# Kernel optimization log

Hardware: AMD Instinct MI355X
Metric: run time of the kernel (lower is better)

Reference implementation:

```python
import jax, jax.numpy as jnp
import numpy as np

B, L, D, H, E, R, FF, K = 4, 1024, 1024, 16, 8, 64, 4096, 2
DH = D // H
EPS = 1e-5
SCALING = 2.0


def layer_norm(x, g, b):
    m = jnp.mean(x, axis=-1, keepdims=True)
    v = jnp.mean(jnp.square(x - m), axis=-1, keepdims=True)
    return (x - m) * jax.lax.rsqrt(v + EPS) * g + b


def setup_inputs() -> dict:
    key = jax.random.key(0)
    ks = jax.random.split(key, 16)
    s = 0.02
    return {
        "hidden_states": jax.random.normal(ks[0], (B, L, D), dtype=jnp.float32),
        "wq": jax.random.normal(ks[1], (D, D), dtype=jnp.float32) * s,
        "wk": jax.random.normal(ks[2], (D, D), dtype=jnp.float32) * s,
        "wv": jax.random.normal(ks[3], (D, D), dtype=jnp.float32) * s,
        "wo": jax.random.normal(ks[4], (D, D), dtype=jnp.float32) * s,
        "bq": jnp.zeros((D,), jnp.float32),
        "bk": jnp.zeros((D,), jnp.float32),
        "bv": jnp.zeros((D,), jnp.float32),
        "bo": jnp.zeros((D,), jnp.float32),
        "ln1_g": jnp.ones((D,), jnp.float32),
        "ln1_b": jnp.zeros((D,), jnp.float32),
        "w1": jax.random.normal(ks[5], (D, FF), dtype=jnp.float32) * s,
        "b1": jnp.zeros((FF,), jnp.float32),
        "w2": jax.random.normal(ks[6], (FF, D), dtype=jnp.float32) * s,
        "b2": jnp.zeros((D,), jnp.float32),
        "ln2_g": jnp.ones((D,), jnp.float32),
        "ln2_b": jnp.zeros((D,), jnp.float32),
        # adapter: dense1 D -> E*R, per-expert dense2 R -> D, gate D -> E
        "adp_w1": jax.random.normal(ks[7], (D, E * R), dtype=jnp.float32) * s,
        "adp_b1": jnp.zeros((E * R,), jnp.float32),
        "adp_w2": jax.random.normal(ks[8], (E, R, D), dtype=jnp.float32) * s,
        "adp_b2": jnp.zeros((E, D), jnp.float32),
        "gate_w": jax.random.normal(ks[9], (D, E), dtype=jnp.float32) * s,
        "gate_b": jnp.zeros((E,), jnp.float32),
    }


def reference(hidden_states, wq, wk, wv, wo, bq, bk, bv, bo, ln1_g, ln1_b,
              w1, b1, w2, b2, ln2_g, ln2_b,
              adp_w1, adp_b1, adp_w2, adp_b2, gate_w, gate_b):
    x = hidden_states
    # --- Roberta self-attention ---
    q = (x @ wq + bq).reshape(B, L, H, DH)
    k = (x @ wk + bk).reshape(B, L, H, DH)
    v = (x @ wv + bv).reshape(B, L, H, DH)
    scores = jnp.einsum("bqhd,bkhd->bhqk", q, k) / jnp.sqrt(jnp.float32(DH))
    probs = jax.nn.softmax(scores, axis=-1)
    ctx = jnp.einsum("bhqk,bkhd->bqhd", probs, v).reshape(B, L, D)
    attn_out = layer_norm(ctx @ wo + bo + x, ln1_g, ln1_b)

    # --- FFN (intermediate + output) ---
    inter = jax.nn.gelu(attn_out @ w1 + b1, approximate=False)
    layer_out = layer_norm(inter @ w2 + b2 + attn_out, ln2_g, ln2_b)

    # --- LoRA_MD_Adapter with NaiveGate (dense compute all experts, then combine) ---
    h = jax.nn.gelu(attn_out @ adp_w1 + adp_b1, approximate=False)  # [B,L,E*R]
    h = h.reshape(B, L, E, R)
    adp = jnp.einsum("bler,erd->bled", h, adp_w2) + adp_b2  # [B,L,E,D]
    logits = attn_out @ gate_w + gate_b  # [B,L,E]
    topv, topi = jax.lax.top_k(logits, K)  # [B,L,K]
    gate_score = jax.nn.softmax(topv, axis=-1)  # [B,L,K]
    # LoRA_MD combine: weight ALL per-expert outputs by top-k softmax scores
    # scattered to the selected experts, then sum over experts.
    picked = jnp.take_along_axis(adp, topi[..., None], axis=2)  # [B,L,K,D]
    adp_out = jnp.sum(picked * gate_score[..., None], axis=2) * SCALING  # [B,L,D]

    return layer_out + adp_out
```

## Files before the change

kernel.cpp:

```cpp
#include <hip/hip_runtime.h>
#include <cstddef>
#include <cstdint>

#define B_   4
#define L_   1024
#define D_   1024
#define H_   16
#define DH_  64
#define E_   8
#define R_   64
#define FF_  4096
#define NTOK (B_ * L_)

typedef __attribute__((ext_vector_type(8))) short bf16x8;
typedef __attribute__((ext_vector_type(4))) float f32x4;
typedef unsigned short us;

__device__ __forceinline__ float gelu_f(float x) {
  return 0.5f * x * (1.0f + erff(x * 0.7071067811865476f));
}

__device__ __forceinline__ us bf16_of(float f) {
  union { float f; uint32_t u; } x; x.f = f;
  uint32_t r = x.u + 0x7FFFu + ((x.u >> 16) & 1u);
  return (us)(r >> 16);
}
__device__ __forceinline__ float f32_of(us h) {
  union { uint32_t u; float f; } x; x.u = ((uint32_t)h) << 16;
  return x.f;
}
__device__ __forceinline__ void split_hl(float v, us& hi, us& lo) {
  hi = bf16_of(v);
  lo = bf16_of(v - f32_of(hi));
}

__device__ __forceinline__ void glds16(const void* g, const void* l) {
  __builtin_amdgcn_global_load_lds(
      (const __attribute__((address_space(1))) unsigned int*)g,
      (__attribute__((address_space(3))) unsigned int*)l, 16, 0, 0);
}

__global__ __launch_bounds__(256)
void fhi(const float* __restrict__ X, us* __restrict__ Hh, int n4) {
  int i = blockIdx.x * 256 + threadIdx.x;
  if (i >= n4) return;
  float4 v = ((const float4*)X)[i];
  ushort4 h = {bf16_of(v.x), bf16_of(v.y), bf16_of(v.z), bf16_of(v.w)};
  ((ushort4*)Hh)[i] = h;
}

__global__ __launch_bounds__(256)
void bconcat(const float* __restrict__ a, const float* __restrict__ b,
             const float* __restrict__ c, float* __restrict__ o) {
  int i = blockIdx.x * 256 + threadIdx.x;
  if (i >= 3072) return;
  o[i] = (i < 1024) ? a[i] : (i < 2048 ? b[i - 1024] : c[i - 2048]);
}

__global__ __launch_bounds__(256)
void wsplit_t(const float* __restrict__ W, us* __restrict__ Th,
              us* __restrict__ Tl, int K, int N) {
  __shared__ float tile[64][65];
  const int k0 = blockIdx.y * 64, n0 = blockIdx.x * 64;
  const int t = threadIdx.x;
  const int r = t >> 4, c4 = (t & 15) * 4;
  #pragma unroll
  for (int p = 0; p < 4; ++p) {
    const int k = r + p * 16;
    *(float4*)&tile[k][c4] = *(const float4*)&W[(size_t)(k0 + k) * N + n0 + c4];
  }
  __syncthreads();
  #pragma unroll
  for (int p = 0; p < 4; ++p) {
    const int n = r + p * 16;
    float v0 = tile[c4 + 0][n], v1 = tile[c4 + 1][n];
    float v2 = tile[c4 + 2][n], v3 = tile[c4 + 3][n];
    ushort4 h, l;
    split_hl(v0, h.x, l.x); split_hl(v1, h.y, l.y);
    split_hl(v2, h.z, l.z); split_hl(v3, h.w, l.w);
    const size_t o = (size_t)(n0 + n) * K + k0 + c4;
    *(ushort4*)&Th[o] = h;
    *(ushort4*)&Tl[o] = l;
  }
}

template<int EPI>
__global__ __launch_bounds__(256, 2)
void gemm_mfma(const us* __restrict__ Ah, const us* __restrict__ Al,
               const us* __restrict__ Bh, const us* __restrict__ Bl,
               const float* __restrict__ bias,
               const float* __restrict__ ResF,
               float* __restrict__ Cf, int M, int N, int K) {
  __shared__ us sAh[128 * 32], sAl[128 * 32];
  __shared__ us sBh[128 * 32], sBl[128 * 32];

  const int t = threadIdx.x;
  const int lane = t & 63;
  const int wid = t >> 6;
  const int wm = wid >> 1, wn = wid & 1;

  const int nwgx = gridDim.x;
  const int nwg = nwgx * gridDim.y;
  const int idl = blockIdx.y * nwgx + blockIdx.x;
  const int swz = (idl & 7) * (nwg >> 3) + (idl >> 3);
  const int m0 = (swz / nwgx) * 128;
  const int n0 = (swz % nwgx) * 128;

  const int srow = wid * 32 + (lane >> 2);
  const int skoff = (lane & 3) * 8;

  f32x4 acc[4][4];
  #pragma unroll
  for (int i = 0; i < 4; ++i)
    #pragma unroll
    for (int j = 0; j < 4; ++j)
      acc[i][j] = (f32x4){0.f, 0.f, 0.f, 0.f};

  const int fr = lane & 15, fq = lane >> 4;

  for (int k0 = 0; k0 < K; k0 += 32) {
    __syncthreads();
    #pragma unroll
    for (int c = 0; c < 2; ++c) {
      const size_t ga = (size_t)(m0 + srow + c * 16) * K + k0 + skoff;
      const size_t gb = (size_t)(n0 + srow + c * 16) * K + k0 + skoff;
      const int ldso = (wid * 32 + c * 16) * 32;
      glds16(Ah + ga, &sAh[ldso]);
      glds16(Al + ga, &sAl[ldso]);
      glds16(Bh + gb, &sBh[ldso]);
      glds16(Bl + gb, &sBl[ldso]);
    }
    __syncthreads();

    bf16x8 ah[4], al[4], bh[4], bl[4];
    #pragma unroll
    for (int i = 0; i < 4; ++i) {
      const int ra = (wm * 64 + i * 16 + fr) * 32 + fq * 8;
      ah[i] = *(const bf16x8*)&sAh[ra];
      al[i] = *(const bf16x8*)&sAl[ra];
      const int rb = (wn * 64 + i * 16 + fr) * 32 + fq * 8;
      bh[i] = *(const bf16x8*)&sBh[rb];
      bl[i] = *(const bf16x8*)&sBl[rb];
    }
    #pragma unroll
    for (int i = 0; i < 4; ++i)
      #pragma unroll
      for (int j = 0; j < 4; ++j) {
        acc[i][j] = __builtin_amdgcn_mfma_f32_16x16x32_bf16(ah[i], bh[j], acc[i][j], 0, 0, 0);
        acc[i][j] = __builtin_amdgcn_mfma_f32_16x16x32_bf16(al[i], bh[j], acc[i][j], 0, 0, 0);
        acc[i][j] = __builtin_amdgcn_mfma_f32_16x16x32_bf16(ah[i], bl[j], acc[i][j], 0, 0, 0);
      }
  }

  float bcol[4];
  #pragma unroll
  for (int j = 0; j < 4; ++j) bcol[j] = bias[n0 + wn * 64 + j * 16 + fr];

  #pragma unroll
  for (int i = 0; i < 4; ++i) {
    #pragma unroll
    for (int r = 0; r < 4; ++r) {
      const int row = m0 + wm * 64 + i * 16 + fq * 4 + r;
      const size_t ro = (size_t)row * N;
      #pragma unroll
      for (int j = 0; j < 4; ++j) {
        const int col = n0 + wn * 64 + j * 16 + fr;
        float v = acc[i][j][r] + bcol[j];
        if (EPI == 1) {
          Cf[ro + col] = gelu_f(v);
        } else if (EPI == 2) {
          Cf[ro + col] = v + ResF[ro + col];
        } else {
          Cf[ro + col] = v;
        }
      }
    }
  }
}

template<int EPI>
__global__ __launch_bounds__(512, 2)
void gemm256(const us* __restrict__ Ah,
             const us* __restrict__ Bh, const us* __restrict__ Bl,
             const float* __restrict__ bias,
             float* __restrict__ Cf, us* __restrict__ Ch, us* __restrict__ Cl,
             us* __restrict__ Kh2, us* __restrict__ Kl2,
             us* __restrict__ Vh2, us* __restrict__ Vl2,
             int M, int N, int Kfull, int klen) {
  __shared__ us sm3[3][3][8192];

  const int t = threadIdx.x;
  const int lane = t & 63, wid = t >> 6;
  const int wm = wid >> 2, wn = wid & 3;
  const int fr = lane & 15, fq = lane >> 4;
  const int rsw8 = (fq ^ ((fr >> 1) & 3)) * 8;

  const int nx = N >> 8;
  const int idl = blockIdx.x + blockIdx.y * nx;
  const int xcd = idl & 7, jj = idl >> 3;
  const int band = (M >> 8) >> 3;
  const int m0 = (xcd * band + (jj % band)) << 8;
  const int n0 = (jj / band) << 8;
  const int koff = blockIdx.z * klen;

  const int srow = t >> 2;
  const int gchunk = (t & 3) ^ ((t >> 3) & 3);
  const int dso = srow * 32 + (t & 3) * 8;

  auto stage1 = [&](int buf, int kt, int idx) {
    const int stream = idx >> 1;
    const int half = idx & 1;
    const us* gp = (stream == 0) ? Ah : (stream == 1 ? Bh : Bl);
    const int rbase = ((stream == 0) ? m0 : n0) + half * 128 + srow;
    const size_t g = (size_t)rbase * Kfull + koff + kt * 32 + gchunk * 8;
    glds16(gp + g, &sm3[buf][stream][half * 4096 + dso]);
  };

  f32x4 acc[8][4];
  #pragma unroll
  for (int i = 0; i < 8; ++i)
    #pragma unroll
    for (int n = 0; n < 4; ++n) acc[i][n] = (f32x4){0.f, 0.f, 0.f, 0.f};

  #pragma unroll
  for (int idx = 0; idx < 6; ++idx) stage1(0, 0, idx);
  #pragma unroll
  for (int idx = 0; idx < 6; ++idx) stage1(1, 1, idx);

  const int nt = klen >> 5;
  for (int g = 0; g < nt; ++g) {
    const int cb = g % 3;
    if (g < nt - 1) { asm volatile("s_waitcnt vmcnt(6)" ::: "memory"); }
    else            { asm volatile("s_waitcnt vmcnt(0)" ::: "memory"); }
    __builtin_amdgcn_sched_barrier(0);
    __builtin_amdgcn_s_barrier();
    __builtin_amdgcn_sched_barrier(0);

    const us* sA  = sm3[cb][0];
    const us* sBh = sm3[cb][1];
    const us* sBl = sm3[cb][2];

    bf16x8 bhf[4], blf[4];
    #pragma unroll
    for (int n = 0; n < 4; ++n) {
      const int rb = (wn * 64 + n * 16 + fr) * 32 + rsw8;
      bhf[n] = *(const bf16x8*)&sBh[rb];
      blf[n] = *(const bf16x8*)&sBl[rb];
    }
    bf16x8 a_cur = *(const bf16x8*)&sA[(wm * 128 + fr) * 32 + rsw8];

    const bool pf = (g + 2 < nt);
    const int nb = (g + 2) % 3;

    #pragma unroll
    for (int i = 0; i < 8; ++i) {
      if (pf && i < 6) stage1(nb, g + 2, i);
      bf16x8 a_nxt;
      if (i < 7) {
        a_nxt = *(const bf16x8*)&sA[(wm * 128 + (i + 1) * 16 + fr) * 32 + rsw8];
        asm volatile("s_waitcnt lgkmcnt(1)" ::: "memory");
      } else {
        asm volatile("s_waitcnt lgkmcnt(0)" ::: "memory");
      }
      __builtin_amdgcn_sched_barrier(0);
      __builtin_amdgcn_s_setprio(1);
      #pragma unroll
      for (int n = 0; n < 4; ++n) {
        acc[i][n] = __builtin_amdgcn_mfma_f32_16x16x32_bf16(a_cur, bhf[n], acc[i][n], 0, 0, 0);
        acc[i][n] = __builtin_amdgcn_mfma_f32_16x16x32_bf16(a_cur, blf[n], acc[i][n], 0, 0, 0);
      }
      __builtin_amdgcn_s_setprio(0);
      if (i < 7) a_cur = a_nxt;
    }
  }

  if (EPI == 12) {
    float* pk = (blockIdx.z == 0) ? Cf :
                (blockIdx.z == 1) ? (float*)Kh2 :
                (blockIdx.z == 2) ? (float*)Kl2 : (float*)Vh2;
    #pragma unroll
    for (int i = 0; i < 8; ++i) {
      #pragma unroll
      for (int r = 0; r < 4; ++r) {
        const int row = m0 + wm * 128 + i * 16 + fq * 4 + r;
        const size_t ro = (size_t)row * N;
        #pragma unroll
        for (int n = 0; n < 4; ++n) {
          const int col = n0 + wn * 64 + n * 16 + fr;
          pk[ro + col] = acc[i][n][r];
        }
      }
    }
    return;
  }

  float bcol[4];
  #pragma unroll
  for (int n = 0; n < 4; ++n) bcol[n] = bias[n0 + wn * 64 + n * 16 + fr];

  if (EPI == 11) {
    #pragma unroll
    for (int i = 0; i < 8; ++i) {
      #pragma unroll
      for (int r = 0; r < 4; ++r) {
        const int row = m0 + wm * 128 + i * 16 + fq * 4 + r;
        const size_t ro = (size_t)row * N;
        #pragma unroll
        for (int n = 0; n < 4; ++n) {
          const int col = n0 + wn * 64 + n * 16 + fr;
          Ch[ro + col] = bf16_of(gelu_f(acc[i][n][r] + bcol[n]));
        }
      }
    }
    return;
  }

  {
    const int sel = n0 >> 10;
    if (sel < 2) {
      us* dh = (sel == 0) ? Ch : Kh2;
      us* dl = (sel == 0) ? Cl : Kl2;
      #pragma unroll
      for (int i = 0; i < 8; ++i) {
        #pragma unroll
        for (int r = 0; r < 4; ++r) {
          const int row = m0 + wm * 128 + i * 16 + fq * 4 + r;
          const size_t ro = (size_t)row * 1024;
          #pragma unroll
          for (int n = 0; n < 4; ++n) {
            const int c10 = (n0 & 1023) + wn * 64 + n * 16 + fr;
            float v = acc[i][n][r] + bcol[n];
            us h, l; split_hl(v, h, l);
            dh[ro + c10] = h; dl[ro + c10] = l;
          }
        }
      }
    } else {
      #pragma unroll
      for (int i = 0; i < 8; ++i) {
        #pragma unroll
        for (int n = 0; n < 4; ++n) {
          const int c10 = (n0 & 1023) + wn * 64 + n * 16 + fr;
          const int hh2 = c10 >> 6, dh = c10 & 63;
          const int row0 = m0 + wm * 128 + i * 16 + fq * 4;
          const int bb = row0 >> 10, ltok = row0 & 1023;
          ushort4 h4, l4;
          float v0 = acc[i][n][0] + bcol[n];
          float v1 = acc[i][n][1] + bcol[n];
          float v2 = acc[i][n][2] + bcol[n];
          float v3 = acc[i][n][3] + bcol[n];
          split_hl(v0, h4.x, l4.x); split_hl(v1, h4.y, l4.y);
          split_hl(v2, h4.z, l4.z); split_hl(v3, h4.w, l4.w);
          const size_t off = ((size_t)(bb * 16 + hh2) * 64 + dh) * L_ + ltok;
          *(ushort4*)&Vh2[off] = h4;
          *(ushort4*)&Vl2[off] = l4;
        }
      }
    }
  }
}

__global__ __launch_bounds__(256, 3)
void attn_mfma(const us* __restrict__ Qh, const us* __restrict__ Ql,
               const us* __restrict__ Kh, const us* __restrict__ Kl,
               const us* __restrict__ Vth, const us* __restrict__ Vtl,
               us* __restrict__ Oh, us* __restrict__ Ol) {
  const int raw = blockIdx.x + blockIdx.y * 16;
  const int hh = (raw & 7) + 8 * ((raw >> 3) >> 4);
  const int qq = (raw >> 3) & 15;
  const int b = hh >> 4, h = hh & 15;

  const int t = threadIdx.x;
  const int w = t >> 6, lane = t & 63;
  const int fr = lane & 15, g = lane >> 4;

  __shared__ __align__(16) unsigned char smem[51200];
  us* sKh = (us*)(smem);
  us* sKl = (us*)(smem + 8192);
  us* sVh = (us*)(smem + 16384);
  us* sVl = (us*)(smem + 24576);
  us* sPh = (us*)(smem + 32768);
  us* sPl = (us*)(smem + 41984);
  float* fb = (float*)smem;

  const int tok0 = b * L_ + qq * 64 + w * 16;
  bf16x8 qfh[2], qfl[2];
  #pragma unroll
  for (int ks = 0; ks < 2; ++ks) {
    const size_t qo = (size_t)(tok0 + fr) * D_ + h * 64 + ks * 32 + g * 8;
    qfh[ks] = *(const bf16x8*)&Qh[qo];
    qfl[ks] = *(const bf16x8*)&Ql[qo];
  }

  float m = -INFINITY, l = 0.0f;
  f32x4 ctx[4];
  #pragma unroll
  for (int i = 0; i < 4; ++i) ctx[i] = (f32x4){0.f, 0.f, 0.f, 0.f};

  for (int kt = 0; kt < 16; ++kt) {
    const int k0 = kt * 64;
    __syncthreads();
    #pragma unroll
    for (int p = 0; p < 2; ++p) {
      const int ci = w * 128 + p * 64 + lane;
      const int dbase = (w * 128 + p * 64) * 8;
      {
        const int ks = ci >> 8, rem = ci & 255, key = rem >> 2, sub = rem & 3;
        const size_t src = (size_t)(b * L_ + k0 + key) * D_ + h * 64 + ks * 32 + sub * 8;
        glds16(Kh + src, sKh + dbase);
        glds16(Kl + src, sKl + dbase);
      }
      {
        const int d = ci >> 3, c = ci & 7;
        const size_t src = (size_t)(hh * 64 + d) * L_ + k0 + ((c ^ (d & 7)) * 8);
        glds16(Vth + src, sVh + dbase);
        glds16(Vtl + src, sVl + dbase);
      }
    }
    __syncthreads();

    f32x4 accS[4];
    #pragma unroll
    for (int i = 0; i < 4; ++i) accS[i] = (f32x4){0.f, 0.f, 0.f, 0.f};
    #pragma unroll
    for (int ks = 0; ks < 2; ++ks) {
      #pragma unroll
      for (int i = 0; i < 4; ++i) {
        const int ra = (ks * 64 + i * 16 + fr) * 32 + g * 8;
        bf16x8 ah = *(const bf16x8*)&sKh[ra];
        bf16x8 al = *(const bf16x8*)&sKl[ra];
        accS[i] = __builtin_amdgcn_mfma_f32_16x16x32_bf16(ah, qfh[ks], accS[i], 0, 0, 0);
        accS[i] = __builtin_amdgcn_mfma_f32_16x16x32_bf16(al, qfh[ks], accS[i], 0, 0, 0);
        accS[i] = __builtin_amdgcn_mfma_f32_16x16x32_bf16(ah, qfl[ks], accS[i], 0, 0, 0);
      }
    }

    float sv[4][4];
    float mloc = -INFINITY;
    #pragma unroll
    for (int i = 0; i < 4; ++i)
      #pragma unroll
      for (int r = 0; r < 4; ++r) {
        sv[i][r] = accS[i][r] * 0.125f;
        mloc = fmaxf(mloc, sv[i][r]);
      }
    mloc = fmaxf(mloc, __shfl_xor(mloc, 16));
    mloc = fmaxf(mloc, __shfl_xor(mloc, 32));
    const float mnew = fmaxf(m, mloc);
    const float alpha = expf(m - mnew);
    float p[4][4];
    float lt = 0.f;
    #pragma unroll
    for (int i = 0; i < 4; ++i)
      #pragma unroll
      for (int r = 0; r < 4; ++r) {
        p[i][r] = expf(sv[i][r] - mnew);
        lt += p[i][r];
      }
    lt += __shfl_xor(lt, 16);
    lt += __shfl_xor(lt, 32);
    l = l * alpha + lt;
    m = mnew;
    #pragma unroll
    for (int i = 0; i < 4; ++i) {
      ctx[i][0] *= alpha; ctx[i][1] *= alpha;
      ctx[i][2] *= alpha; ctx[i][3] *= alpha;
    }

    #pragma unroll
    for (int i = 0; i < 4; ++i) {
      us h0 = bf16_of(p[i][0]), h1 = bf16_of(p[i][1]);
      us h2 = bf16_of(p[i][2]), h3 = bf16_of(p[i][3]);
      uint2 hv = {(uint32_t)h0 | ((uint32_t)h1 << 16),
                  (uint32_t)h2 | ((uint32_t)h3 << 16)};
      us l0 = bf16_of(p[i][0] - f32_of(h0)), l1 = bf16_of(p[i][1] - f32_of(h1));
      us l2 = bf16_of(p[i][2] - f32_of(h2)), l3 = bf16_of(p[i][3] - f32_of(h3));
      uint2 lv = {(uint32_t)l0 | ((uint32_t)l1 << 16),
                  (uint32_t)l2 | ((uint32_t)l3 << 16)};
      const int po = (w * 16 + fr) * 72 + i * 16 + g * 4;
      *(uint2*)&sPh[po] = hv;
      *(uint2*)&sPl[po] = lv;
    }

    #pragma unroll
    for (int ks = 0; ks < 2; ++ks) {
      const int pb = (w * 16 + fr) * 72 + ks * 32 + g * 8;
      bf16x8 pah = *(const bf16x8*)&sPh[pb];
      bf16x8 pal = *(const bf16x8*)&sPl[pb];
      #pragma unroll
      for (int i = 0; i < 4; ++i) {
        const int d = i * 16 + fr;
        const int pc = (ks * 4 + g) ^ (d & 7);
        bf16x8 vh = *(const bf16x8*)&sVh[d * 64 + pc * 8];
        bf16x8 vl = *(const bf16x8*)&sVl[d * 64 + pc * 8];
        ctx[i] = __builtin_amdgcn_mfma_f32_16x16x32_bf16(vh, pah, ctx[i], 0, 0, 0);
        ctx[i] = __builtin_amdgcn_mfma_f32_16x16x32_bf16(vl, pah, ctx[i], 0, 0, 0);
        ctx[i] = __builtin_amdgcn_mfma_f32_16x16x32_bf16(vh, pal, ctx[i], 0, 0, 0);
      }
    }
  }

  const float invl = 1.0f / l;
  __syncthreads();
  #pragma unroll
  for (int i = 0; i < 4; ++i)
    #pragma unroll
    for (int r = 0; r < 4; ++r)
      fb[(i * 16 + g * 4 + r) * 64 + w * 16 + fr] = ctx[i][r] * invl;
  __syncthreads();

  {
    const int q = t >> 2, dg = t & 3;
    const size_t ob = (size_t)(b * L_ + qq * 64 + q) * D_ + h * 64;
    #pragma unroll
    for (int u = 0; u < 4; ++u) {
      const int d0 = dg * 16 + u * 4;
      ushort4 h4, l4;
      float v0 = fb[(d0 + 0) * 64 + q];
      float v1 = fb[(d0 + 1) * 64 + q];
      float v2 = fb[(d0 + 2) * 64 + q];
      float v3 = fb[(d0 + 3) * 64 + q];
      split_hl(v0, h4.x, l4.x); split_hl(v1, h4.y, l4.y);
      split_hl(v2, h4.z, l4.z); split_hl(v3, h4.w, l4.w);
      *(ushort4*)&Oh[ob + d0] = h4;
      *(ushort4*)&Ol[ob + d0] = l4;
    }
  }
}

template<int MODE>
__global__ __launch_bounds__(256)
void layernorm_k(const float* __restrict__ X, const float* __restrict__ g,
                 const float* __restrict__ b, float* __restrict__ Yf,
                 us* __restrict__ Yh, us* __restrict__ Yl) {
  const int row = blockIdx.x;
  const int t = threadIdx.x;
  const float* x = X + (size_t)row * D_;

  float4 v = *(const float4*)&x[t * 4];
  float s  = v.x + v.y + v.z + v.w;
  float ss = v.x * v.x + v.y * v.y + v.z * v.z + v.w * v.w;

  #pragma unroll
  for (int off = 1; off < 64; off <<= 1) {
    s  += __shfl_xor(s, off);
    ss += __shfl_xor(ss, off);
  }
  __shared__ float red[4][2];
  const int wid = t >> 6;
  if ((t & 63) == 0) { red[wid][0] = s; red[wid][1] = ss; }
  __syncthreads();
  s  = red[0][0] + red[1][0] + red[2][0] + red[3][0];
  ss = red[0][1] + red[1][1] + red[2][1] + red[3][1];

  const float mean = s * (1.0f / D_);
  const float var  = ss * (1.0f / D_) - mean * mean;
  const float inv  = rsqrtf(var + 1e-5f);

  float4 gv = *(const float4*)&g[t * 4];
  float4 bv = *(const float4*)&b[t * 4];
  float4 o;
  o.x = (v.x - mean) * inv * gv.x + bv.x;
  o.y = (v.y - mean) * inv * gv.y + bv.y;
  o.z = (v.z - mean) * inv * gv.z + bv.z;
  o.w = (v.w - mean) * inv * gv.w + bv.w;
  if (MODE == 0) {
    *(float4*)&Yf[(size_t)row * D_ + t * 4] = o;
  } else {
    ushort4 h, l;
    split_hl(o.x, h.x, l.x); split_hl(o.y, h.y, l.y);
    split_hl(o.z, h.z, l.z); split_hl(o.w, h.w, l.w);
    *(ushort4*)&Yh[(size_t)row * D_ + t * 4] = h;
    *(ushort4*)&Yl[(size_t)row * D_ + t * 4] = l;
  }
}

__global__ __launch_bounds__(256)
void lnred4(const float* __restrict__ P0, const float* __restrict__ P1,
            const float* __restrict__ P2, const float* __restrict__ P3,
            const float* __restrict__ b2,
            const us* __restrict__ Rh, const us* __restrict__ Rl,
            const float* __restrict__ g, const float* __restrict__ be,
            float* __restrict__ Y) {
  const int row = blockIdx.x;
  const int t = threadIdx.x;
  const size_t o = (size_t)row * D_ + t * 4;

  float4 v0 = *(const float4*)&P0[o];
  float4 v1 = *(const float4*)&P1[o];
  float4 v2 = *(const float4*)&P2[o];
  float4 v3 = *(const float4*)&P3[o];
  float4 bb = *(const float4*)&b2[t * 4];
  ushort4 rh = *(const ushort4*)&Rh[o];
  ushort4 rl = *(const ushort4*)&Rl[o];
  float4 v;
  v.x = v0.x + v1.x + v2.x + v3.x + bb.x + f32_of(rh.x) + f32_of(rl.x);
  v.y = v0.y + v1.y + v2.y + v3.y + bb.y + f32_of(rh.y) + f32_of(rl.y);
  v.z = v0.z + v1.z + v2.z + v3.z + bb.z + f32_of(rh.z) + f32_of(rl.z);
  v.w = v0.w + v1.w + v2.w + v3.w + bb.w + f32_of(rh.w) + f32_of(rl.w);

  float s  = v.x + v.y + v.z + v.w;
  float ss = v.x * v.x + v.y * v.y + v.z * v.z + v.w * v.w;
  #pragma unroll
  for (int off = 1; off < 64; off <<= 1) {
    s  += __shfl_xor(s, off);
    ss += __shfl_xor(ss, off);
  }
  __shared__ float red[4][2];
  const int wid = t >> 6;
  if ((t & 63) == 0) { red[wid][0] = s; red[wid][1] = ss; }
  __syncthreads();
  s  = red[0][0] + red[1][0] + red[2][0] + red[3][0];
  ss = red[0][1] + red[1][1] + red[2][1] + red[3][1];

  const float mean = s * (1.0f / D_);
  const float var  = ss * (1.0f / D_) - mean * mean;
  const float inv  = rsqrtf(var + 1e-5f);

  float4 gv = *(const float4*)&g[t * 4];
  float4 bv = *(const float4*)&be[t * 4];
  float4 y;
  y.x = (v.x - mean) * inv * gv.x + bv.x;
  y.y = (v.y - mean) * inv * gv.y + bv.y;
  y.z = (v.z - mean) * inv * gv.z + bv.z;
  y.w = (v.w - mean) * inv * gv.w + bv.w;
  *(float4*)&Y[o] = y;
}

__global__ __launch_bounds__(256)
void adapter_combine_hl(const us* __restrict__ Xh, const us* __restrict__ Xl,
                        const float* __restrict__ Hall,
                        const float* __restrict__ Lout,
                        const us* __restrict__ W2b,
                        const float* __restrict__ B2,
                        const float* __restrict__ GW,
                        const float* __restrict__ GB,
                        float* __restrict__ Out) {
  const int tok = blockIdx.x;
  const int t = threadIdx.x;

  __shared__ float xs[D_];
  __shared__ float part[256];
  __shared__ float logit_s[E_];
  __shared__ float hs[2 * R_];
  __shared__ int   e_sh[2];
  __shared__ float g_sh[2];

  {
    ushort4 h = *(const ushort4*)&Xh[(size_t)tok * D_ + t * 4];
    ushort4 l = *(const ushort4*)&Xl[(size_t)tok * D_ + t * 4];
    xs[t * 4 + 0] = f32_of(h.x) + f32_of(l.x);
    xs[t * 4 + 1] = f32_of(h.y) + f32_of(l.y);
    xs[t * 4 + 2] = f32_of(h.z) + f32_of(l.z);
    xs[t * 4 + 3] = f32_of(h.w) + f32_of(l.w);
  }
  __syncthreads();

  {
    const int e = t & 7, seg = t >> 3;
    float p = 0.f;
    #pragma unroll 8
    for (int i = 0; i < 32; ++i) {
      const int d = seg * 32 + i;
      p = fmaf(xs[d], GW[d * E_ + e], p);
    }
    part[t] = p;
  }
  __syncthreads();
  if (t < E_) {
    float s = GB[t];
    for (int sg = 0; sg < 32; ++sg) s += part[sg * 8 + t];
    logit_s[t] = s;
  }
  __syncthreads();
  if (t == 0) {
    int e1 = 0; float v1 = logit_s[0];
    for (int i = 1; i < E_; ++i) if (logit_s[i] > v1) { v1 = logit_s[i]; e1 = i; }
    int e2 = -1; float v2 = -INFINITY;
    for (int i = 0; i < E_; ++i) if (i != e1 && logit_s[i] > v2) { v2 = logit_s[i]; e2 = i; }
    const float ee = expf(v2 - v1);
    const float den = 1.0f + ee;
    g_sh[0] = 1.0f / den; g_sh[1] = ee / den;
    e_sh[0] = e1; e_sh[1] = e2;
  }
  __syncthreads();
  const int e1 = e_sh[0], e2 = e_sh[1];
  const float g1 = g_sh[0], g2 = g_sh[1];

  if (t < 2 * R_) {
    const int ex = (t < R_) ? e1 : e2;
    const int r = t & (R_ - 1);
    hs[t] = Hall[(size_t)tok * (E_ * R_) + ex * R_ + r];
  }
  __syncthreads();

  const int d = t * 4;
  float4 b1v = *(const float4*)&B2[e1 * D_ + d];
  float4 b2v = *(const float4*)&B2[e2 * D_ + d];
  float4 acc;
  acc.x = g1 * b1v.x + g2 * b2v.x;
  acc.y = g1 * b1v.y + g2 * b2v.y;
  acc.z = g1 * b1v.z + g2 * b2v.z;
  acc.w = g1 * b1v.w + g2 * b2v.w;

  #pragma unroll 8
  for (int r = 0; r < R_; ++r) {
    const float f = g1 * hs[r];
    ushort4 w = *(const ushort4*)&W2b[((size_t)e1 * R_ + r) * D_ + d];
    acc.x = fmaf(f, f32_of(w.x), acc.x); acc.y = fmaf(f, f32_of(w.y), acc.y);
    acc.z = fmaf(f, f32_of(w.z), acc.z); acc.w = fmaf(f, f32_of(w.w), acc.w);
  }
  #pragma unroll 8
  for (int r = 0; r < R_; ++r) {
    const float f = g2 * hs[R_ + r];
    ushort4 w = *(const ushort4*)&W2b[((size_t)e2 * R_ + r) * D_ + d];
    acc.x = fmaf(f, f32_of(w.x), acc.x); acc.y = fmaf(f, f32_of(w.y), acc.y);
    acc.z = fmaf(f, f32_of(w.z), acc.z); acc.w = fmaf(f, f32_of(w.w), acc.w);
  }

  float4 lo = *(const float4*)&Lout[(size_t)tok * D_ + d];
  float4 o = {lo.x + 2.0f * acc.x, lo.y + 2.0f * acc.y,
              lo.z + 2.0f * acc.z, lo.w + 2.0f * acc.w};
  *(float4*)&Out[(size_t)tok * D_ + d] = o;
}

extern "C" void kernel_launch(void* const* d_in, const int* in_sizes, int n_in,
                              void* d_out, int out_size, void* d_ws, size_t ws_size,
                              hipStream_t stream) {
  const float* x     = (const float*)d_in[0];
  const float* wq    = (const float*)d_in[1];
  const float* wk    = (const float*)d_in[2];
  const float* wv    = (const float*)d_in[3];
  const float* wo    = (const float*)d_in[4];
  const float* bq    = (const float*)d_in[5];
  const float* bk    = (const float*)d_in[6];
  const float* bv    = (const float*)d_in[7];
  const float* bo    = (const float*)d_in[8];
  const float* ln1g  = (const float*)d_in[9];
  const float* ln1b  = (const float*)d_in[10];
  const float* w1    = (const float*)d_in[11];
  const float* b1    = (const float*)d_in[12];
  const float* w2    = (const float*)d_in[13];
  const float* b2    = (const float*)d_in[14];
  const float* ln2g  = (const float*)d_in[15];
  const float* ln2b  = (const float*)d_in[16];
  const float* aw1   = (const float*)d_in[17];
  const float* ab1   = (const float*)d_in[18];
  const float* aw2   = (const float*)d_in[19];
  const float* ab2   = (const float*)d_in[20];
  const float* gw    = (const float*)d_in[21];
  const float* gb    = (const float*)d_in[22];
  float* out = (float*)d_out;

  char* base = (char*)d_ws;
  const size_t MB = 1ull << 20;

  us* qkvTh = (us*)(base + 0 * MB);  us* qkvTl = (us*)(base + 6 * MB);
  us* woTh  = (us*)(base + 12 * MB); us* woTl  = (us*)(base + 14 * MB);
  us* w1Th  = (us*)(base + 16 * MB); us* w1Tl  = (us*)(base + 24 * MB);
  us* w2Th  = (us*)(base + 32 * MB); us* w2Tl  = (us*)(base + 40 * MB);
  us* a1Th  = (us*)(base + 48 * MB); us* a1Tl  = (us*)(base + 49 * MB);
  us* w2b   = (us*)(base + 50 * MB);
  float* bqkv = (float*)(base + 51 * MB);
  us* xh   = (us*)(base + 52 * MB);
  us* ctxh = (us*)(base + 52 * MB);  us* ctxl = (us*)(base + 60 * MB);
  us* qbh  = (us*)(base + 68 * MB);  us* qbl  = (us*)(base + 76 * MB);
  us* kbh  = (us*)(base + 84 * MB);  us* kbl  = (us*)(base + 92 * MB);
  us* vth  = (us*)(base + 100 * MB); us* vtl  = (us*)(base + 108 * MB);
  float* ATTNPRE = (float*)(base + 68 * MB);
  us* aoh  = (us*)(base + 84 * MB);  us* aol  = (us*)(base + 92 * MB);
  us* inth = (us*)(base + 116 * MB);
  float* P0 = (float*)(base + 52 * MB);
  float* P1 = (float*)(base + 68 * MB);
  float* P2 = (float*)(base + 100 * MB);
  float* P3 = (float*)(base + 148 * MB);
  float* LOUT = P0;
  float* HALL = (float*)(base + 68 * MB);

  const dim3 blk(256);
  const us* nu = nullptr;
  const float* nf = nullptr;

  fhi<<<dim3(NTOK * D_ / 1024), blk, 0, stream>>>(x, xh, NTOK * D_ / 4);
  wsplit_t<<<dim3(16, 16), blk, 0, stream>>>(wq, qkvTh, qkvTl, D_, D_);
  wsplit_t<<<dim3(16, 16), blk, 0, stream>>>(wk, qkvTh + 1024 * 1024, qkvTl + 1024 * 1024, D_, D_);
  wsplit_t<<<dim3(16, 16), blk, 0, stream>>>(wv, qkvTh + 2048 * 1024, qkvTl + 2048 * 1024, D_, D_);
  wsplit_t<<<dim3(16, 16), blk, 0, stream>>>(wo, woTh, woTl, D_, D_);
  wsplit_t<<<dim3(64, 16), blk, 0, stream>>>(w1, w1Th, w1Tl, D_, FF_);
  wsplit_t<<<dim3(16, 64), blk, 0, stream>>>(w2, w2Th, w2Tl, FF_, D_);
  wsplit_t<<<dim3(8, 16),  blk, 0, stream>>>(aw1, a1Th, a1Tl, D_, E_ * R_);
  fhi<<<dim3(E_ * R_ * D_ / 1024), blk, 0, stream>>>(aw2, w2b, E_ * R_ * D_ / 4);
  bconcat<<<dim3(12), blk, 0, stream>>>(bq, bk, bv, bqkv);

  gemm256<10><<<dim3(12, 16), dim3(512), 0, stream>>>(
      xh, qkvTh, qkvTl, bqkv, nullptr, qbh, qbl, kbh, kbl, vth, vtl,
      NTOK, 3072, D_, D_);
  attn_mfma<<<dim3(16, 64), blk, 0, stream>>>(qbh, qbl, kbh, kbl, vth, vtl, ctxh, ctxl);
  gemm_mfma<2><<<dim3(8, 32), blk, 0, stream>>>(ctxh, ctxl, woTh, woTl, bo, x,
                                                ATTNPRE, NTOK, D_, D_);
  layernorm_k<1><<<dim3(NTOK), blk, 0, stream>>>(ATTNPRE, ln1g, ln1b, nullptr, aoh, aol);
  gemm256<11><<<dim3(16, 16), dim3(512), 0, stream>>>(
      aoh, w1Th, w1Tl, b1, nullptr, inth, nullptr, nullptr, nullptr, nullptr, nullptr,
      NTOK, FF_, D_, D_);
  gemm256<12><<<dim3(4, 16, 4), dim3(512), 0, stream>>>(
      inth, w2Th, w2Tl, nf, P0, nullptr, nullptr, (us*)P1, (us*)P2, (us*)P3, nullptr,
      NTOK, D_, FF_, 1024);
  lnred4<<<dim3(NTOK), blk, 0, stream>>>(P0, P1, P2, P3, b2, aoh, aol, ln2g, ln2b, LOUT);
  gemm_mfma<1><<<dim3(4, 32), blk, 0, stream>>>(aoh, aol, a1Th, a1Tl, ab1, nf,
                                                HALL, NTOK, E_ * R_, D_);
  adapter_combine_hl<<<dim3(NTOK), blk, 0, stream>>>(aoh, aol, HALL, LOUT, w2b, ab2, gw, gb, out);
}
```

Before: 635.2 us.

## Drop low-half bf16 terms in attention and 128-tile GEMMs, add triple-buffered pipelining

Replaces the 128x128 GEMM with a triple-buffered, swizzled, prefetching version that uses only the high bf16 half of the A operand, which cuts its MFMA count from three to two per tile. Attention now reads K and writes ctx as single bf16, drops the low half of P, switches to exp2 with a folded scale, and cuts shared memory to allow higher occupancy. The gemm256 inner loop is restructured to load A fragments in pairs. Every dropped low-half term lowers the precision of the split-bf16 emulation of fp32, which risks tolerance failures.

```diff
diff --git a/kernel.cpp b/kernel.cpp
--- a/kernel.cpp
+++ b/kernel.cpp
@@ -86,75 +86,97 @@
 
 template<int EPI>
 __global__ __launch_bounds__(256, 2)
-void gemm_mfma(const us* __restrict__ Ah, const us* __restrict__ Al,
-               const us* __restrict__ Bh, const us* __restrict__ Bl,
-               const float* __restrict__ bias,
-               const float* __restrict__ ResF,
-               float* __restrict__ Cf, int M, int N, int K) {
-  __shared__ us sAh[128 * 32], sAl[128 * 32];
-  __shared__ us sBh[128 * 32], sBl[128 * 32];
+void gemm128(const us* __restrict__ Ah,
+             const us* __restrict__ Bh, const us* __restrict__ Bl,
+             const float* __restrict__ bias, const float* __restrict__ ResF,
+             float* __restrict__ Cf, int M, int N, int K) {
+  __shared__ us sm3[3][3][4096];
 
   const int t = threadIdx.x;
-  const int lane = t & 63;
-  const int wid = t >> 6;
+  const int lane = t & 63, wid = t >> 6;
   const int wm = wid >> 1, wn = wid & 1;
-
-  const int nwgx = gridDim.x;
-  const int nwg = nwgx * gridDim.y;
-  const int idl = blockIdx.y * nwgx + blockIdx.x;
-  const int swz = (idl & 7) * (nwg >> 3) + (idl >> 3);
-  const int m0 = (swz / nwgx) * 128;
-  const int n0 = (swz % nwgx) * 128;
-
-  const int srow = wid * 32 + (lane >> 2);
-  const int skoff = (lane & 3) * 8;
+  const int fr = lane & 15, fq = lane >> 4;
+  const int rsw8 = (fq ^ ((fr >> 1) & 3)) * 8;
+
+  const int nx = N >> 7;
+  const int idl = blockIdx.x + blockIdx.y * nx;
+  const int xcd = idl & 7, jj = idl >> 3;
+  const int band = (M >> 7) >> 3;
+  const int m0 = (xcd * band + (jj % band)) << 7;
+  const int n0 = (jj / band) << 7;
+
+  const int srow = t >> 2;
+  const int gsub = t & 3;
+
+  auto stage1 = [&](int buf, int kt, int idx) {
+    const int stream = idx >> 1;
+    const int half = idx & 1;
+    const us* gp = (stream == 0) ? Ah : (stream == 1 ? Bh : Bl);
+    const int row = half * 64 + srow;
+    const int gchunk = gsub ^ ((row >> 1) & 3);
+    const int rbase = ((stream == 0) ? m0 : n0) + row;
+    const size_t g = (size_t)rbase * K + kt * 32 + gchunk * 8;
+    glds16(gp + g, &sm3[buf][stream][row * 32 + gsub * 8]);
+  };
 
   f32x4 acc[4][4];
   #pragma unroll
   for (int i = 0; i < 4; ++i)
     #pragma unroll
-    for (int j = 0; j < 4; ++j)
-      acc[i][j] = (f32x4){0.f, 0.f, 0.f, 0.f};
-
-  const int fr = lane & 15, fq = lane >> 4;
-
-  for (int k0 = 0; k0 < K; k0 += 32) {
-    __syncthreads();
-    #pragma unroll
-    for (int c = 0; c < 2; ++c) {
-      const size_t ga = (size_t)(m0 + srow + c * 16) * K + k0 + skoff;
-      const size_t gb = (size_t)(n0 + srow + c * 16) * K + k0 + skoff;
-      const int ldso = (wid * 32 + c * 16) * 32;
-      glds16(Ah + ga, &sAh[ldso]);
-      glds16(Al + ga, &sAl[ldso]);
-      glds16(Bh + gb, &sBh[ldso]);
-      glds16(Bl + gb, &sBl[ldso]);
-    }
-    __syncthreads();
-
-    bf16x8 ah[4], al[4], bh[4], bl[4];
+    for (int n = 0; n < 4; ++n) acc[i][n] = (f32x4){0.f, 0.f, 0.f, 0.f};
+
+  #pragma unroll
+  for (int idx = 0; idx < 6; ++idx) stage1(0, 0, idx);
+  #pragma unroll
+  for (int idx = 0; idx < 6; ++idx) stage1(1, 1, idx);
+
+  const int nt = K >> 5;
+  for (int g = 0; g < nt; ++g) {
+    const int cb = g % 3;
+    if (g < nt - 1) { asm volatile("s_waitcnt vmcnt(6)" ::: "memory"); }
+    else            { asm volatile("s_waitcnt vmcnt(0)" ::: "memory"); }
+    __builtin_amdgcn_sched_barrier(0);
+    __builtin_amdgcn_s_barrier();
+    __builtin_amdgcn_sched_barrier(0);
+
+    const us* sA   = sm3[cb][0];
+    const us* sBh_ = sm3[cb][1];
+    const us* sBl_ = sm3[cb][2];
+
+    bf16x8 bh[4], bl[4], av[4];
+    #pragma unroll
+    for (int n = 0; n < 4; ++n) {
+      const int rb = (wn * 64 + n * 16 + fr) * 32 + rsw8;
+      bh[n] = *(const bf16x8*)&sBh_[rb];
+      bl[n] = *(const bf16x8*)&sBl_[rb];
+    }
+    #pragma unroll
+    for (int i = 0; i < 4; ++i)
+      av[i] = *(const bf16x8*)&sA[(wm * 64 + i * 16 + fr) * 32 + rsw8];
+
+    const bool pf = (g + 2 < nt);
+    const int nb = (g + 2) % 3;
+
     #pragma unroll
     for (int i = 0; i < 4; ++i) {
-      const int ra = (wm * 64 + i * 16 + fr) * 32 + fq * 8;
-      ah[i] = *(const bf16x8*)&sAh[ra];
-      al[i] = *(const bf16x8*)&sAl[ra];
-      const int rb = (wn * 64 + i * 16 + fr) * 32 + fq * 8;
-      bh[i] = *(const bf16x8*)&sBh[rb];
-      bl[i] = *(const bf16x8*)&sBl[rb];
-    }
-    #pragma unroll
-    for (int i = 0; i < 4; ++i)
-      #pragma unroll
-      for (int j = 0; j < 4; ++j) {
-        acc[i][j] = __builtin_amdgcn_mfma_f32_16x16x32_bf16(ah[i], bh[j], acc[i][j], 0, 0, 0);
-        acc[i][j] = __builtin_amdgcn_mfma_f32_16x16x32_bf16(al[i], bh[j], acc[i][j], 0, 0, 0);
-        acc[i][j] = __builtin_amdgcn_mfma_f32_16x16x32_bf16(ah[i], bl[j], acc[i][j], 0, 0, 0);
-      }
+      if (pf && i < 3) { stage1(nb, g + 2, 2 * i); stage1(nb, g + 2, 2 * i + 1); }
+      if (i == 0) {
+        asm volatile("s_waitcnt lgkmcnt(0)" ::: "memory");
+        __builtin_amdgcn_sched_barrier(0);
+      }
+      __builtin_amdgcn_s_setprio(1);
+      #pragma unroll
+      for (int n = 0; n < 4; ++n) {
+        acc[i][n] = __builtin_amdgcn_mfma_f32_16x16x32_bf16(av[i], bh[n], acc[i][n], 0, 0, 0);
+        acc[i][n] = __builtin_amdgcn_mfma_f32_16x16x32_bf16(av[i], bl[n], acc[i][n], 0, 0, 0);
+      }
+      __builtin_amdgcn_s_setprio(0);
+    }
   }
 
   float bcol[4];
   #pragma unroll
-  for (int j = 0; j < 4; ++j) bcol[j] = bias[n0 + wn * 64 + j * 16 + fr];
+  for (int n = 0; n < 4; ++n) bcol[n] = bias[n0 + wn * 64 + n * 16 + fr];
 
   #pragma unroll
   for (int i = 0; i < 4; ++i) {
@@ -163,16 +185,11 @@
       const int row = m0 + wm * 64 + i * 16 + fq * 4 + r;
       const size_t ro = (size_t)row * N;
       #pragma unroll
-      for (int j = 0; j < 4; ++j) {
-        const int col = n0 + wn * 64 + j * 16 + fr;
-        float v = acc[i][j][r] + bcol[j];
-        if (EPI == 1) {
-          Cf[ro + col] = gelu_f(v);
-        } else if (EPI == 2) {
-          Cf[ro + col] = v + ResF[ro + col];
-        } else {
-          Cf[ro + col] = v;
-        }
+      for (int n = 0; n < 4; ++n) {
+        const int col = n0 + wn * 64 + n * 16 + fr;
+        float v = acc[i][n][r] + bcol[n];
+        if (EPI == 1) Cf[ro + col] = gelu_f(v);
+        else          Cf[ro + col] = v + ResF[ro + col];
       }
     }
   }
@@ -228,6 +245,25 @@
   for (int idx = 0; idx < 6; ++idx) stage1(1, 1, idx);
 
   const int nt = klen >> 5;
+  bf16x8 bhf[4], blf[4];
+
+#define PH_MFMA(qq)                                                              \
+  {                                                                              \
+    bf16x8 a0 = *(const bf16x8*)&sm3[cb][0][(wm * 128 + (2*qq) * 16 + fr) * 32 + rsw8];   \
+    bf16x8 a1 = *(const bf16x8*)&sm3[cb][0][(wm * 128 + (2*qq+1) * 16 + fr) * 32 + rsw8]; \
+    asm volatile("s_waitcnt lgkmcnt(0)" ::: "memory");                           \
+    __builtin_amdgcn_sched_barrier(0);                                           \
+    __builtin_amdgcn_s_setprio(1);                                               \
+    _Pragma("unroll")                                                            \
+    for (int n = 0; n < 4; ++n) {                                                \
+      acc[2*qq][n]   = __builtin_amdgcn_mfma_f32_16x16x32_bf16(a0, bhf[n], acc[2*qq][n], 0,0,0);   \
+      acc[2*qq][n]   = __builtin_amdgcn_mfma_f32_16x16x32_bf16(a0, blf[n], acc[2*qq][n], 0,0,0);   \
+      acc[2*qq+1][n] = __builtin_amdgcn_mfma_f32_16x16x32_bf16(a1, bhf[n], acc[2*qq+1][n], 0,0,0); \
+      acc[2*qq+1][n] = __builtin_amdgcn_mfma_f32_16x16x32_bf16(a1, blf[n], acc[2*qq+1][n], 0,0,0); \
+    }                                                                            \
+    __builtin_amdgcn_s_setprio(0);                                               \
+  }
+
   for (int g = 0; g < nt; ++g) {
     const int cb = g % 3;
     if (g < nt - 1) { asm volatile("s_waitcnt vmcnt(6)" ::: "memory"); }
@@ -235,44 +271,23 @@
     __builtin_amdgcn_sched_barrier(0);
     __builtin_amdgcn_s_barrier();
     __builtin_amdgcn_sched_barrier(0);
-
-    const us* sA  = sm3[cb][0];
-    const us* sBh = sm3[cb][1];
-    const us* sBl = sm3[cb][2];
-
-    bf16x8 bhf[4], blf[4];
     #pragma unroll
     for (int n = 0; n < 4; ++n) {
       const int rb = (wn * 64 + n * 16 + fr) * 32 + rsw8;
-      bhf[n] = *(const bf16x8*)&sBh[rb];
-      blf[n] = *(const bf16x8*)&sBl[rb];
-    }
-    bf16x8 a_cur = *(const bf16x8*)&sA[(wm * 128 + fr) * 32 + rsw8];
-
+      bhf[n] = *(const bf16x8*)&sm3[cb][1][rb];
+      blf[n] = *(const bf16x8*)&sm3[cb][2][rb];
+    }
     const bool pf = (g + 2 < nt);
     const int nb = (g + 2) % 3;
-
-    #pragma unroll
-    for (int i = 0; i < 8; ++i) {
-      if (pf && i < 6) stage1(nb, g + 2, i);
-      bf16x8 a_nxt;
-      if (i < 7) {
-        a_nxt = *(const bf16x8*)&sA[(wm * 128 + (i + 1) * 16 + fr) * 32 + rsw8];
-        asm volatile("s_waitcnt lgkmcnt(1)" ::: "memory");
-      } else {
-        asm volatile("s_waitcnt lgkmcnt(0)" ::: "memory");
-      }
-      __builtin_amdgcn_sched_barrier(0);
-      __builtin_amdgcn_s_setprio(1);
-      #pragma unroll
-      for (int n = 0; n < 4; ++n) {
-        acc[i][n] = __builtin_amdgcn_mfma_f32_16x16x32_bf16(a_cur, bhf[n], acc[i][n], 0, 0, 0);
-        acc[i][n] = __builtin_amdgcn_mfma_f32_16x16x32_bf16(a_cur, blf[n], acc[i][n], 0, 0, 0);
-      }
-      __builtin_amdgcn_s_setprio(0);
-      if (i < 7) a_cur = a_nxt;
-    }
-  }
+    if (pf) { stage1(nb, g + 2, 0); stage1(nb, g + 2, 1); }
+    PH_MFMA(0)
+    if (pf) { stage1(nb, g + 2, 2); stage1(nb, g + 2, 3); }
+    PH_MFMA(1)
+    if (pf) { stage1(nb, g + 2, 4); stage1(nb, g + 2, 5); }
+    PH_MFMA(2)
+    PH_MFMA(3)
+  }
+#undef PH_MFMA
 
   if (EPI == 12) {
     float* pk = (blockIdx.z == 0) ? Cf :
@@ -319,7 +334,7 @@
     const int sel = n0 >> 10;
     if (sel < 2) {
       us* dh = (sel == 0) ? Ch : Kh2;
-      us* dl = (sel == 0) ? Cl : Kl2;
+      us* dl = Cl;
       #pragma unroll
       for (int i = 0; i < 8; ++i) {
         #pragma unroll
@@ -330,8 +345,12 @@
           for (int n = 0; n < 4; ++n) {
             const int c10 = (n0 & 1023) + wn * 64 + n * 16 + fr;
             float v = acc[i][n][r] + bcol[n];
-            us h, l; split_hl(v, h, l);
-            dh[ro + c10] = h; dl[ro + c10] = l;
+            if (sel == 0) {
+              us h, l; split_hl(v, h, l);
+              dh[ro + c10] = h; dl[ro + c10] = l;
+            } else {
+              dh[ro + c10] = bf16_of(v);
+            }
           }
         }
       }
@@ -360,11 +379,11 @@
   }
 }
 
-__global__ __launch_bounds__(256, 3)
+__global__ __launch_bounds__(256, 4)
 void attn_mfma(const us* __restrict__ Qh, const us* __restrict__ Ql,
-               const us* __restrict__ Kh, const us* __restrict__ Kl,
+               const us* __restrict__ Kh,
                const us* __restrict__ Vth, const us* __restrict__ Vtl,
-               us* __restrict__ Oh, us* __restrict__ Ol) {
+               us* __restrict__ Oh) {
   const int raw = blockIdx.x + blockIdx.y * 16;
   const int hh = (raw & 7) + 8 * ((raw >> 3) >> 4);
   const int qq = (raw >> 3) & 15;
@@ -374,15 +393,14 @@
   const int w = t >> 6, lane = t & 63;
   const int fr = lane & 15, g = lane >> 4;
 
-  __shared__ __align__(16) unsigned char smem[51200];
-  us* sKh = (us*)(smem);
-  us* sKl = (us*)(smem + 8192);
-  us* sVh = (us*)(smem + 16384);
-  us* sVl = (us*)(smem + 24576);
-  us* sPh = (us*)(smem + 32768);
-  us* sPl = (us*)(smem + 41984);
+  __shared__ __align__(16) unsigned char smem[33792];
+  us* sK  = (us*)(smem);
+  us* sVh = (us*)(smem + 8192);
+  us* sVl = (us*)(smem + 16384);
+  us* sP  = (us*)(smem + 24576);
   float* fb = (float*)smem;
 
+  const size_t base = ((size_t)b * L_) * D_ + (size_t)h * DH_;
   const int tok0 = b * L_ + qq * 64 + w * 16;
   bf16x8 qfh[2], qfl[2];
   #pragma unroll
@@ -392,10 +410,12 @@
     qfl[ks] = *(const bf16x8*)&Ql[qo];
   }
 
+  const float Cc = 0.18033688011112042f;
   float m = -INFINITY, l = 0.0f;
   f32x4 ctx[4];
   #pragma unroll
   for (int i = 0; i < 4; ++i) ctx[i] = (f32x4){0.f, 0.f, 0.f, 0.f};
+  const int rswk = (g ^ ((fr >> 1) & 3)) * 8;
 
   for (int kt = 0; kt < 16; ++kt) {
     const int k0 = kt * 64;
@@ -403,18 +423,17 @@
     #pragma unroll
     for (int p = 0; p < 2; ++p) {
       const int ci = w * 128 + p * 64 + lane;
-      const int dbase = (w * 128 + p * 64) * 8;
+      const int db = ci * 8;
       {
         const int ks = ci >> 8, rem = ci & 255, key = rem >> 2, sub = rem & 3;
-        const size_t src = (size_t)(b * L_ + k0 + key) * D_ + h * 64 + ks * 32 + sub * 8;
-        glds16(Kh + src, sKh + dbase);
-        glds16(Kl + src, sKl + dbase);
+        const int subp = sub ^ ((key >> 1) & 3);
+        glds16(Kh + base + (size_t)(k0 + key) * D_ + ks * 32 + subp * 8, sK + db);
       }
       {
         const int d = ci >> 3, c = ci & 7;
         const size_t src = (size_t)(hh * 64 + d) * L_ + k0 + ((c ^ (d & 7)) * 8);
-        glds16(Vth + src, sVh + dbase);
-        glds16(Vtl + src, sVl + dbase);
+        glds16(Vth + src, sVh + db);
+        glds16(Vtl + src, sVl + db);
       }
     }
     __syncthreads();
@@ -426,36 +445,33 @@
     for (int ks = 0; ks < 2; ++ks) {
       #pragma unroll
       for (int i = 0; i < 4; ++i) {
-        const int ra = (ks * 64 + i * 16 + fr) * 32 + g * 8;
-        bf16x8 ah = *(const bf16x8*)&sKh[ra];
-        bf16x8 al = *(const bf16x8*)&sKl[ra];
-        accS[i] = __builtin_amdgcn_mfma_f32_16x16x32_bf16(ah, qfh[ks], accS[i], 0, 0, 0);
-        accS[i] = __builtin_amdgcn_mfma_f32_16x16x32_bf16(al, qfh[ks], accS[i], 0, 0, 0);
-        accS[i] = __builtin_amdgcn_mfma_f32_16x16x32_bf16(ah, qfl[ks], accS[i], 0, 0, 0);
-      }
-    }
-
-    float sv[4][4];
+        const int ra = (ks * 64 + i * 16 + fr) * 32 + rswk;
+        bf16x8 a = *(const bf16x8*)&sK[ra];
+        accS[i] = __builtin_amdgcn_mfma_f32_16x16x32_bf16(a, qfh[ks], accS[i], 0, 0, 0);
+        accS[i] = __builtin_amdgcn_mfma_f32_16x16x32_bf16(a, qfl[ks], accS[i], 0, 0, 0);
+      }
+    }
+
+    float p4[4][4];
     float mloc = -INFINITY;
     #pragma unroll
     for (int i = 0; i < 4; ++i)
       #pragma unroll
       for (int r = 0; r < 4; ++r) {
-        sv[i][r] = accS[i][r] * 0.125f;
-        mloc = fmaxf(mloc, sv[i][r]);
+        p4[i][r] = accS[i][r] * Cc;
+        mloc = fmaxf(mloc, p4[i][r]);
       }
     mloc = fmaxf(mloc, __shfl_xor(mloc, 16));
     mloc = fmaxf(mloc, __shfl_xor(mloc, 32));
     const float mnew = fmaxf(m, mloc);
-    const float alpha = expf(m - mnew);
-    float p[4][4];
+    const float alpha = exp2f(m - mnew);
     float lt = 0.f;
     #pragma unroll
     for (int i = 0; i < 4; ++i)
       #pragma unroll
       for (int r = 0; r < 4; ++r) {
-        p[i][r] = expf(sv[i][r] - mnew);
-        lt += p[i][r];
+        p4[i][r] = exp2f(p4[i][r] - mnew);
+        lt += p4[i][r];
       }
     lt += __shfl_xor(lt, 16);
     lt += __shfl_xor(lt, 32);
@@ -469,33 +485,25 @@
 
     #pragma unroll
     for (int i = 0; i < 4; ++i) {
-      us h0 = bf16_of(p[i][0]), h1 = bf16_of(p[i][1]);
-      us h2 = bf16_of(p[i][2]), h3 = bf16_of(p[i][3]);
+      us h0 = bf16_of(p4[i][0]), h1 = bf16_of(p4[i][1]);
+      us h2 = bf16_of(p4[i][2]), h3 = bf16_of(p4[i][3]);
       uint2 hv = {(uint32_t)h0 | ((uint32_t)h1 << 16),
                   (uint32_t)h2 | ((uint32_t)h3 << 16)};
-      us l0 = bf16_of(p[i][0] - f32_of(h0)), l1 = bf16_of(p[i][1] - f32_of(h1));
-      us l2 = bf16_of(p[i][2] - f32_of(h2)), l3 = bf16_of(p[i][3] - f32_of(h3));
-      uint2 lv = {(uint32_t)l0 | ((uint32_t)l1 << 16),
-                  (uint32_t)l2 | ((uint32_t)l3 << 16)};
-      const int po = (w * 16 + fr) * 72 + i * 16 + g * 4;
-      *(uint2*)&sPh[po] = hv;
-      *(uint2*)&sPl[po] = lv;
+      *(uint2*)&sP[(w * 16 + fr) * 72 + i * 16 + g * 4] = hv;
     }
 
     #pragma unroll
     for (int ks = 0; ks < 2; ++ks) {
       const int pb = (w * 16 + fr) * 72 + ks * 32 + g * 8;
-      bf16x8 pah = *(const bf16x8*)&sPh[pb];
-      bf16x8 pal = *(const bf16x8*)&sPl[pb];
+      bf16x8 pa = *(const bf16x8*)&sP[pb];
       #pragma unroll
       for (int i = 0; i < 4; ++i) {
         const int d = i * 16 + fr;
         const int pc = (ks * 4 + g) ^ (d & 7);
         bf16x8 vh = *(const bf16x8*)&sVh[d * 64 + pc * 8];
         bf16x8 vl = *(const bf16x8*)&sVl[d * 64 + pc * 8];
-        ctx[i] = __builtin_amdgcn_mfma_f32_16x16x32_bf16(vh, pah, ctx[i], 0, 0, 0);
-        ctx[i] = __builtin_amdgcn_mfma_f32_16x16x32_bf16(vl, pah, ctx[i], 0, 0, 0);
-        ctx[i] = __builtin_amdgcn_mfma_f32_16x16x32_bf16(vh, pal, ctx[i], 0, 0, 0);
+        ctx[i] = __builtin_amdgcn_mfma_f32_16x16x32_bf16(vh, pa, ctx[i], 0, 0, 0);
+        ctx[i] = __builtin_amdgcn_mfma_f32_16x16x32_bf16(vl, pa, ctx[i], 0, 0, 0);
       }
     }
   }
@@ -515,15 +523,11 @@
     #pragma unroll
     for (int u = 0; u < 4; ++u) {
       const int d0 = dg * 16 + u * 4;
-      ushort4 h4, l4;
-      float v0 = fb[(d0 + 0) * 64 + q];
-      float v1 = fb[(d0 + 1) * 64 + q];
-      float v2 = fb[(d0 + 2) * 64 + q];
-      float v3 = fb[(d0 + 3) * 64 + q];
-      split_hl(v0, h4.x, l4.x); split_hl(v1, h4.y, l4.y);
-      split_hl(v2, h4.z, l4.z); split_hl(v3, h4.w, l4.w);
+      ushort4 h4 = {bf16_of(fb[(d0 + 0) * 64 + q]),
+                    bf16_of(fb[(d0 + 1) * 64 + q]),
+                    bf16_of(fb[(d0 + 2) * 64 + q]),
+                    bf16_of(fb[(d0 + 3) * 64 + q])};
       *(ushort4*)&Oh[ob + d0] = h4;
-      *(ushort4*)&Ol[ob + d0] = l4;
     }
   }
 }
@@ -763,9 +767,9 @@
   us* w2b   = (us*)(base + 50 * MB);
   float* bqkv = (float*)(base + 51 * MB);
   us* xh   = (us*)(base + 52 * MB);
-  us* ctxh = (us*)(base + 52 * MB);  us* ctxl = (us*)(base + 60 * MB);
+  us* ctxh = (us*)(base + 52 * MB);
   us* qbh  = (us*)(base + 68 * MB);  us* qbl  = (us*)(base + 76 * MB);
-  us* kbh  = (us*)(base + 84 * MB);  us* kbl  = (us*)(base + 92 * MB);
+  us* kbh  = (us*)(base + 84 * MB);
   us* vth  = (us*)(base + 100 * MB); us* vtl  = (us*)(base + 108 * MB);
   float* ATTNPRE = (float*)(base + 68 * MB);
   us* aoh  = (us*)(base + 84 * MB);  us* aol  = (us*)(base + 92 * MB);
@@ -793,11 +797,11 @@
   bconcat<<<dim3(12), blk, 0, stream>>>(bq, bk, bv, bqkv);
 
   gemm256<10><<<dim3(12, 16), dim3(512), 0, stream>>>(
-      xh, qkvTh, qkvTl, bqkv, nullptr, qbh, qbl, kbh, kbl, vth, vtl,
+      xh, qkvTh, qkvTl, bqkv, nullptr, qbh, qbl, kbh, nullptr, vth, vtl,
       NTOK, 3072, D_, D_);
-  attn_mfma<<<dim3(16, 64), blk, 0, stream>>>(qbh, qbl, kbh, kbl, vth, vtl, ctxh, ctxl);
-  gemm_mfma<2><<<dim3(8, 32), blk, 0, stream>>>(ctxh, ctxl, woTh, woTl, bo, x,
-                                                ATTNPRE, NTOK, D_, D_);
+  attn_mfma<<<dim3(16, 64), blk, 0, stream>>>(qbh, qbl, kbh, vth, vtl, ctxh);
+  gemm128<2><<<dim3(8, 32), blk, 0, stream>>>(ctxh, woTh, woTl, bo, x,
+                                              ATTNPRE, NTOK, D_, D_);
   layernorm_k<1><<<dim3(NTOK), blk, 0, stream>>>(ATTNPRE, ln1g, ln1b, nullptr, aoh, aol);
   gemm256<11><<<dim3(16, 16), dim3(512), 0, stream>>>(
       aoh, w1Th, w1Tl, b1, nullptr, inth, nullptr, nullptr, nullptr, nullptr, nullptr,
@@ -806,7 +810,7 @@
       inth, w2Th, w2Tl, nf, P0, nullptr, nullptr, (us*)P1, (us*)P2, (us*)P3, nullptr,
       NTOK, D_, FF_, 1024);
   lnred4<<<dim3(NTOK), blk, 0, stream>>>(P0, P1, P2, P3, b2, aoh, aol, ln2g, ln2b, LOUT);
-  gemm_mfma<1><<<dim3(4, 32), blk, 0, stream>>>(aoh, aol, a1Th, a1Tl, ab1, nf,
-                                                HALL, NTOK, E_ * R_, D_);
+  gemm128<1><<<dim3(4, 32), blk, 0, stream>>>(aoh, a1Th, a1Tl, ab1, nf,
+                                              HALL, NTOK, E_ * R_, D_);
   adapter_combine_hl<<<dim3(NTOK), blk, 0, stream>>>(aoh, aol, HALL, LOUT, w2b, ab2, gw, gb, out);
 }
```

After: 571.4 us. 10.0% less time.
